# Kernel tuning notes

Hardware: AMD Instinct MI355X
Metric: run time of the kernel (lower is better)

## Reference

```python
import jax, jax.numpy as jnp
import numpy as np

NUM_HEADS = 16

def setup_inputs() -> dict:
    key = jax.random.key(0)
    ks = jax.random.split(key, 5)
    b, n, d = 2, 2048, 1024
    s = 0.02
    return {
        "x": jax.random.normal(ks[0], (b, n, d), jnp.float32),
        "wq": jax.random.normal(ks[1], (d, d), jnp.float32) * s,
        "wk": jax.random.normal(ks[2], (d, d), jnp.float32) * s,
        "wv": jax.random.normal(ks[3], (d, d), jnp.float32) * s,
        "wo": jax.random.normal(ks[4], (d, d), jnp.float32) * s,
        "bo": jnp.zeros((d,), jnp.float32),
    }

def reference(x, wq, wk, wv, wo, bo):
    b, n, c = x.shape
    h = NUM_HEADS
    hd = c // h
    scale = hd ** -0.5
    # qkv projections (qkv_bias=False); torch Linear computes x @ W.T
    def split_heads(t):
        return t.reshape(b, n, h, hd).transpose(0, 2, 1, 3)  # b h n d
    q = split_heads(x @ wq.T)
    k = split_heads(x @ wk.T)
    v = split_heads(x @ wv.T)
    dots = jnp.einsum('bhid,bhjd->bhij', q, k) * scale
    attn = jax.nn.softmax(dots, axis=-1)  # attn_drop=0 -> identity
    out = jnp.einsum('bhij,bhjd->bhid', attn, v)
    out = out.transpose(0, 2, 1, 3).reshape(b, n, c)
    out = out @ wo.T + bo  # proj_drop=0 -> identity
    return out
```

## Files before the change

kernel.cpp:

```cpp
#include <hip/hip_runtime.h>
#include <hip/hip_bf16.h>

typedef float f32x4 __attribute__((ext_vector_type(4)));
typedef short short8 __attribute__((ext_vector_type(8)));
typedef short short4v __attribute__((ext_vector_type(4)));

#define MFMA(a, b, c) __builtin_amdgcn_mfma_f32_16x16x32_bf16((a), (b), (c), 0, 0, 0)

#if __has_builtin(__builtin_amdgcn_exp2f)
#define EXP2(x) __builtin_amdgcn_exp2f(x)
#else
#define EXP2(x) exp2f(x)
#endif

#define B_  2
#define N_  2048
#define C_  1024
#define H_  16
#define HD_ 64
#define M_  (B_ * N_)

#define QSCALE 0.18033688011112042f

typedef const __attribute__((address_space(1))) void* gp_t;
typedef __attribute__((address_space(3))) void* sp_t;
#define GLL16(g, s) __builtin_amdgcn_global_load_lds((gp_t)(const void*)(g), (sp_t)(void*)(s), 16, 0, 0)

__device__ __forceinline__ short f2bf(float f) {
    union { float fv; unsigned u; } v; v.fv = f;
    unsigned r = v.u + 0x7fffu + ((v.u >> 16) & 1u);
    return (short)(r >> 16);
}
__device__ __forceinline__ unsigned pack_rne(float a, float b) {
    return (unsigned)(unsigned short)f2bf(a) | ((unsigned)(unsigned short)f2bf(b) << 16);
}

__global__ __launch_bounds__(256) void convert_kernel(
    const float* __restrict__ x,  const float* __restrict__ wq,
    const float* __restrict__ wk, const float* __restrict__ wv,
    const float* __restrict__ wo, short* __restrict__ dst)
{
    size_t e = ((size_t)blockIdx.x * 256 + threadIdx.x) * 8;
    const float* src; size_t off;
    if (e < 4194304)      { src = x;  off = e; }
    else if (e < 5242880) { src = wq; off = e - 4194304; }
    else if (e < 6291456) { src = wk; off = e - 5242880; }
    else if (e < 7340032) { src = wv; off = e - 6291456; }
    else                  { src = wo; off = e - 7340032; }
    float4 a = *(const float4*)(src + off);
    float4 b = *(const float4*)(src + off + 4);
    short8 s;
    s[0] = f2bf(a.x); s[1] = f2bf(a.y); s[2] = f2bf(a.z); s[3] = f2bf(a.w);
    s[4] = f2bf(b.x); s[5] = f2bf(b.y); s[6] = f2bf(b.z); s[7] = f2bf(b.w);
    *(short8*)(dst + e) = s;
}

__global__ __launch_bounds__(256) void qkv_gemm(
    const short* __restrict__ xb, const short* __restrict__ Wb,
    short* __restrict__ Qb, short* __restrict__ Kb, short* __restrict__ Vt)
{
    const int m0 = blockIdx.x * 128;
    const int n0 = blockIdx.y * 128;
    __shared__ short As[128 * 64];
    __shared__ short Bs[128 * 64];
    const int tid  = threadIdx.x;
    const int wave = tid >> 6, lane = tid & 63;
    const int quad = lane >> 4, l16 = lane & 15;
    const int wr = (wave >> 1) * 64, wc = (wave & 1) * 64;
    const int sw = l16 & 7;

    const int rS = tid >> 3;
    const int cS = (tid & 7) ^ (rS & 7);
    const short* A_src = xb + (size_t)(m0 + rS) * C_ + cS * 8;
    const short* B_src = Wb + (size_t)(n0 + rS) * C_ + cS * 8;

    f32x4 acc[4][4] = {};

    for (int kk = 0; kk < C_; kk += 64) {
        __syncthreads();
        #pragma unroll
        for (int it = 0; it < 4; ++it) {
            GLL16(A_src + (size_t)(it * 32) * C_ + kk, &As[it * 2048 + tid * 8]);
            GLL16(B_src + (size_t)(it * 32) * C_ + kk, &Bs[it * 2048 + tid * 8]);
        }
        __syncthreads();
        short8 af[4][2], bf[4][2];
        #pragma unroll
        for (int mi = 0; mi < 4; ++mi) {
            int row = (wr + mi * 16 + l16) * 64;
            af[mi][0] = *(const short8*)&As[row + ((quad    ) ^ sw) * 8];
            af[mi][1] = *(const short8*)&As[row + ((quad + 4) ^ sw) * 8];
        }
        #pragma unroll
        for (int ni = 0; ni < 4; ++ni) {
            int row = (wc + ni * 16 + l16) * 64;
            bf[ni][0] = *(const short8*)&Bs[row + ((quad    ) ^ sw) * 8];
            bf[ni][1] = *(const short8*)&Bs[row + ((quad + 4) ^ sw) * 8];
        }
        #pragma unroll
        for (int k2 = 0; k2 < 2; ++k2)
        #pragma unroll
        for (int mi = 0; mi < 4; ++mi)
        #pragma unroll
        for (int ni = 0; ni < 4; ++ni)
            acc[mi][ni] = MFMA(af[mi][k2], bf[ni][k2], acc[mi][ni]);
    }

    const int which = n0 >> 10;
    const int nb = n0 & 1023;
    #pragma unroll
    for (int mi = 0; mi < 4; ++mi)
    #pragma unroll
    for (int ni = 0; ni < 4; ++ni)
    #pragma unroll
    for (int r = 0; r < 4; ++r) {
        int m  = m0 + wr + mi * 16 + quad * 4 + r;
        int cc = nb + wc + ni * 16 + l16;
        float av = acc[mi][ni][r];
        if (which == 0) av *= QSCALE;
        short bv = f2bf(av);
        int bb = m >> 11, ns = m & (N_ - 1);
        int h = cc >> 6, d = cc & 63;
        size_t bh = (size_t)(bb * H_ + h);
        if (which == 0)      Qb[(bh * N_ + ns) * HD_ + d] = bv;
        else if (which == 1) Kb[(bh * N_ + ns) * HD_ + d] = bv;
        else                 Vt[(bh * HD_ + d) * N_ + ns] = bv;
    }
}

__global__ __launch_bounds__(256, 5) void attn_split(
    const short* __restrict__ Qb, const short* __restrict__ Kb,
    const short* __restrict__ Vt, float* __restrict__ Opart,
    float* __restrict__ lpart)
{
    const int bid = blockIdx.x;
    const int swz = (bid & 7) * 256 + (bid >> 3);
    const int bh = swz >> 6;
    const int i0 = ((swz >> 1) & 31) * 64;
    const int sp = swz & 1;
    __shared__ short Ks[2][64 * 64];
    __shared__ short Vs[2][64 * 64];
    const int tid  = threadIdx.x;
    const int wave = tid >> 6, lane = tid & 63;
    const int quad = lane >> 4, l16 = lane & 15;
    const int sw = l16 & 7;

    const short* Qg = Qb + ((size_t)bh * N_ + i0) * HD_;
    const short* Kg = Kb + (size_t)bh * N_ * HD_;
    const short* Vg = Vt + (size_t)bh * HD_ * N_;

    const int row0 = tid >> 3,  c0 = (tid & 7) ^ (row0 & 7);
    const int row1 = row0 + 32, c1 = (tid & 7) ^ (row1 & 7);
    const short* KgA0 = Kg + (sp * 1024 + row0) * HD_ + c0 * 8;
    const short* KgA1 = Kg + (sp * 1024 + row1) * HD_ + c1 * 8;
    const short* VgA0 = Vg + (size_t)row0 * N_ + sp * 1024 + c0 * 8;
    const short* VgA1 = Vg + (size_t)row1 * N_ + sp * 1024 + c1 * 8;

    short8 qf[2];
    {
        const short* qrow = Qg + (wave * 16 + l16) * HD_;
        qf[0] = *(const short8*)(qrow + quad * 8);
        qf[1] = *(const short8*)(qrow + quad * 8 + 32);
    }

    GLL16(KgA0, &Ks[0][tid * 8]);
    GLL16(KgA1, &Ks[0][(tid + 256) * 8]);
    GLL16(VgA0, &Vs[0][tid * 8]);
    GLL16(VgA1, &Vs[0][(tid + 256) * 8]);
    __syncthreads();

    f32x4 o[4] = {};
    float lrow = 0.f;

    for (int jt = 0; jt < 16; ++jt) {
        const int cur = jt & 1;
        if (jt + 1 < 16) {
            int j1 = (jt + 1) * 64;
            GLL16(KgA0 + (size_t)j1 * HD_, &Ks[cur ^ 1][tid * 8]);
            GLL16(KgA1 + (size_t)j1 * HD_, &Ks[cur ^ 1][(tid + 256) * 8]);
            GLL16(VgA0 + j1, &Vs[cur ^ 1][tid * 8]);
            GLL16(VgA1 + j1, &Vs[cur ^ 1][(tid + 256) * 8]);
        }
        const short* Kc = Ks[cur];
        const short* Vc = Vs[cur];

        #pragma unroll
        for (int half = 0; half < 2; ++half) {
            unsigned pq[4];
            #pragma unroll
            for (int nio = 0; nio < 2; ++nio) {
                int ni = half * 2 + nio;
                int krow = (ni * 16 + l16) * 64;
                short8 kf0 = *(const short8*)&Kc[krow + ((quad ^ sw) * 8)];
                short8 kf1 = *(const short8*)&Kc[krow + (((quad + 4) ^ sw) * 8)];
                f32x4 st = {0.f, 0.f, 0.f, 0.f};
                __builtin_amdgcn_s_setprio(1);
                st = MFMA(kf0, qf[0], st);
                st = MFMA(kf1, qf[1], st);
                __builtin_amdgcn_s_setprio(0);
                union { float f; unsigned u; } e0, e1, e2, e3;
                e0.f = EXP2(st[0]); e1.f = EXP2(st[1]);
                e2.f = EXP2(st[2]); e3.f = EXP2(st[3]);
                lrow += (e0.f + e1.f) + (e2.f + e3.f);
                pq[nio * 2]     = __builtin_amdgcn_perm(e1.u, e0.u, 0x07060302u);
                pq[nio * 2 + 1] = __builtin_amdgcn_perm(e3.u, e2.u, 0x07060302u);
            }
            #pragma unroll
            for (int di = 0; di < 4; ++di) {
                int vrow = (di * 16 + l16) * 64;
                int ch1 = (half * 4 +     (quad >> 1)) ^ sw;
                int ch2 = (half * 4 + 2 + (quad >> 1)) ^ sw;
                union { struct { short4v lo, hi; } p; short8 v; } va;
                va.p.lo = *(const short4v*)&Vc[vrow + ch1 * 8 + (quad & 1) * 4];
                va.p.hi = *(const short4v*)&Vc[vrow + ch2 * 8 + (quad & 1) * 4];
                union { unsigned u[4]; short8 v; } pb;
                pb.u[0] = pq[0]; pb.u[1] = pq[1];
                pb.u[2] = pq[2]; pb.u[3] = pq[3];
                __builtin_amdgcn_s_setprio(1);
                o[di] = MFMA(va.v, pb.v, o[di]);
                __builtin_amdgcn_s_setprio(0);
            }
        }
        __syncthreads();
    }

    {
        float l = lrow;
        l += __shfl_xor(l, 16, 64);
        l += __shfl_xor(l, 32, 64);
        int ig = i0 + wave * 16 + l16;
        float* obase = Opart + ((size_t)(sp * 32 + bh) * N_ + ig) * HD_;
        #pragma unroll
        for (int di = 0; di < 4; ++di)
            *(f32x4*)(obase + di * 16 + quad * 4) = o[di];
        if (quad == 0) lpart[sp * 65536 + bh * N_ + ig] = l;
    }
}

__global__ __launch_bounds__(256) void merge_kernel(
    const float* __restrict__ Opart, const float* __restrict__ lpart,
    short* __restrict__ Ob)
{
    int e8 = (blockIdx.x * 256 + threadIdx.x) * 8;
    int bh = e8 >> 17;
    int rem = e8 & 131071;
    int ig = rem >> 6, d = rem & 63;
    f32x4 a0 = *(const f32x4*)(Opart + e8);
    f32x4 a1 = *(const f32x4*)(Opart + e8 + 4);
    f32x4 b0 = *(const f32x4*)(Opart + 4194304 + e8);
    f32x4 b1 = *(const f32x4*)(Opart + 4194304 + e8 + 4);
    float inv = 1.f / (lpart[bh * N_ + ig] + lpart[65536 + bh * N_ + ig]);
    short8 s;
    s[0] = f2bf((a0[0] + b0[0]) * inv); s[1] = f2bf((a0[1] + b0[1]) * inv);
    s[2] = f2bf((a0[2] + b0[2]) * inv); s[3] = f2bf((a0[3] + b0[3]) * inv);
    s[4] = f2bf((a1[0] + b1[0]) * inv); s[5] = f2bf((a1[1] + b1[1]) * inv);
    s[6] = f2bf((a1[2] + b1[2]) * inv); s[7] = f2bf((a1[3] + b1[3]) * inv);
    int b = bh >> 4, h = bh & (H_ - 1);
    *(short8*)&Ob[((size_t)(b * N_ + ig)) * C_ + h * HD_ + d] = s;
}

__global__ __launch_bounds__(256) void proj_gemm(
    const short* __restrict__ Ob, const short* __restrict__ wob,
    const float* __restrict__ bo, float* __restrict__ out)
{
    const int m0 = blockIdx.x * 64;
    const int n0 = blockIdx.y * 128;
    __shared__ short As[64 * 64];
    __shared__ short Bs[128 * 64];
    const int tid  = threadIdx.x;
    const int wave = tid >> 6, lane = tid & 63;
    const int quad = lane >> 4, l16 = lane & 15;
    const int wr = (wave >> 1) * 32, wc = (wave & 1) * 64;
    const int sw = l16 & 7;

    const int rS = tid >> 3;
    const int cS = (tid & 7) ^ (rS & 7);
    const short* A_src = Ob  + (size_t)(m0 + rS) * C_ + cS * 8;
    const short* B_src = wob + (size_t)(n0 + rS) * C_ + cS * 8;

    f32x4 acc[2][4] = {};

    for (int kk = 0; kk < C_; kk += 64) {
        __syncthreads();
        GLL16(A_src + kk, &As[tid * 8]);
        GLL16(A_src + (size_t)32 * C_ + kk, &As[(tid + 256) * 8]);
        #pragma unroll
        for (int it = 0; it < 4; ++it)
            GLL16(B_src + (size_t)(it * 32) * C_ + kk, &Bs[it * 2048 + tid * 8]);
        __syncthreads();
        short8 af[2][2], bf[4][2];
        #pragma unroll
        for (int mi = 0; mi < 2; ++mi) {
            int row = (wr + mi * 16 + l16) * 64;
            af[mi][0] = *(const short8*)&As[row + ((quad    ) ^ sw) * 8];
            af[mi][1] = *(const short8*)&As[row + ((quad + 4) ^ sw) * 8];
        }
        #pragma unroll
        for (int ni = 0; ni < 4; ++ni) {
            int row = (wc + ni * 16 + l16) * 64;
            bf[ni][0] = *(const short8*)&Bs[row + ((quad    ) ^ sw) * 8];
            bf[ni][1] = *(const short8*)&Bs[row + ((quad + 4) ^ sw) * 8];
        }
        #pragma unroll
        for (int k2 = 0; k2 < 2; ++k2)
        #pragma unroll
        for (int mi = 0; mi < 2; ++mi)
        #pragma unroll
        for (int ni = 0; ni < 4; ++ni)
            acc[mi][ni] = MFMA(af[mi][k2], bf[ni][k2], acc[mi][ni]);
    }

    #pragma unroll
    for (int mi = 0; mi < 2; ++mi)
    #pragma unroll
    for (int ni = 0; ni < 4; ++ni)
    #pragma unroll
    for (int r = 0; r < 4; ++r) {
        int m = m0 + wr + mi * 16 + quad * 4 + r;
        int c = n0 + wc + ni * 16 + l16;
        out[(size_t)m * C_ + c] = acc[mi][ni][r] + bo[c];
    }
}

extern "C" void kernel_launch(void* const* d_in, const int* in_sizes, int n_in,
                              void* d_out, int out_size, void* d_ws, size_t ws_size,
                              hipStream_t stream) {
    const float* x  = (const float*)d_in[0];
    const float* wq = (const float*)d_in[1];
    const float* wk = (const float*)d_in[2];
    const float* wv = (const float*)d_in[3];
    const float* wo = (const float*)d_in[4];
    const float* bo = (const float*)d_in[5];
    float* out = (float*)d_out;

    short* xb  = (short*)d_ws;
    short* Wb  = xb  + 4194304;
    short* wob = Wb  + 3145728;
    short* Qb  = wob + 1048576;
    short* Kb  = Qb  + 4194304;
    short* Vt  = Kb  + 4194304;
    short* Obuf= Vt  + 4194304;
    float* Opart = (float*)(Obuf + 4194304);
    float* lpart = Opart + 2 * 4194304;

    dim3 blk(256);
    convert_kernel<<<4096, blk, 0, stream>>>(x, wq, wk, wv, wo, xb);
    qkv_gemm<<<dim3(M_ / 128, 3072 / 128), blk, 0, stream>>>(xb, Wb, Qb, Kb, Vt);
    attn_split<<<2048, blk, 0, stream>>>(Qb, Kb, Vt, Opart, lpart);
    merge_kernel<<<2048, blk, 0, stream>>>(Opart, lpart, Obuf);
    proj_gemm<<<dim3(M_ / 64, C_ / 128), blk, 0, stream>>>(Obuf, wob, bo, out);
}
```

Baseline: 197.0 us.

## Process two 16-row query subtiles per wave to reuse K/V fragments

Each wave in the split attention kernel now handles 32 query rows (two 16-row subtiles) instead of 16, so each block covers 128 query rows and the grid shrinks from 2048 to 1024 blocks. K and V fragments read from shared memory are reused across both subtiles. This halves the global-to-LDS traffic for K/V per query row and the number of LDS fragment reads per MFMA. In exchange it raises register pressure (occupancy hint lowered from 5 to 4) and leaves fewer blocks to fill the GPU.

```diff
diff --git a/kernel.cpp b/kernel.cpp
--- a/kernel.cpp
+++ b/kernel.cpp
@@ -128,15 +128,15 @@
     }
 }
 
-__global__ __launch_bounds__(256, 5) void attn_split(
+__global__ __launch_bounds__(256, 4) void attn_split(
     const short* __restrict__ Qb, const short* __restrict__ Kb,
     const short* __restrict__ Vt, float* __restrict__ Opart,
     float* __restrict__ lpart)
 {
     const int bid = blockIdx.x;
-    const int swz = (bid & 7) * 256 + (bid >> 3);
-    const int bh = swz >> 6;
-    const int i0 = ((swz >> 1) & 31) * 64;
+    const int swz = (bid & 7) * 128 + (bid >> 3);
+    const int bh = swz >> 5;
+    const int i0 = ((swz >> 1) & 15) * 128;
     const int sp = swz & 1;
     __shared__ short Ks[2][64 * 64];
     __shared__ short Vs[2][64 * 64];
@@ -156,11 +156,12 @@
     const short* VgA0 = Vg + (size_t)row0 * N_ + sp * 1024 + c0 * 8;
     const short* VgA1 = Vg + (size_t)row1 * N_ + sp * 1024 + c1 * 8;
 
-    short8 qf[2];
-    {
-        const short* qrow = Qg + (wave * 16 + l16) * HD_;
-        qf[0] = *(const short8*)(qrow + quad * 8);
-        qf[1] = *(const short8*)(qrow + quad * 8 + 32);
+    short8 qf[2][2];
+    #pragma unroll
+    for (int s = 0; s < 2; ++s) {
+        const short* qrow = Qg + (wave * 32 + s * 16 + l16) * HD_;
+        qf[s][0] = *(const short8*)(qrow + quad * 8);
+        qf[s][1] = *(const short8*)(qrow + quad * 8 + 32);
     }
 
     GLL16(KgA0, &Ks[0][tid * 8]);
@@ -169,8 +170,8 @@
     GLL16(VgA1, &Vs[0][(tid + 256) * 8]);
     __syncthreads();
 
-    f32x4 o[4] = {};
-    float lrow = 0.f;
+    f32x4 o[2][4] = {};
+    float lrow[2] = {0.f, 0.f};
 
     for (int jt = 0; jt < 16; ++jt) {
         const int cur = jt & 1;
@@ -186,24 +187,27 @@
 
         #pragma unroll
         for (int half = 0; half < 2; ++half) {
-            unsigned pq[4];
+            unsigned pq[2][4];
             #pragma unroll
             for (int nio = 0; nio < 2; ++nio) {
                 int ni = half * 2 + nio;
                 int krow = (ni * 16 + l16) * 64;
                 short8 kf0 = *(const short8*)&Kc[krow + ((quad ^ sw) * 8)];
                 short8 kf1 = *(const short8*)&Kc[krow + (((quad + 4) ^ sw) * 8)];
-                f32x4 st = {0.f, 0.f, 0.f, 0.f};
-                __builtin_amdgcn_s_setprio(1);
-                st = MFMA(kf0, qf[0], st);
-                st = MFMA(kf1, qf[1], st);
-                __builtin_amdgcn_s_setprio(0);
-                union { float f; unsigned u; } e0, e1, e2, e3;
-                e0.f = EXP2(st[0]); e1.f = EXP2(st[1]);
-                e2.f = EXP2(st[2]); e3.f = EXP2(st[3]);
-                lrow += (e0.f + e1.f) + (e2.f + e3.f);
-                pq[nio * 2]     = __builtin_amdgcn_perm(e1.u, e0.u, 0x07060302u);
-                pq[nio * 2 + 1] = __builtin_amdgcn_perm(e3.u, e2.u, 0x07060302u);
+                #pragma unroll
+                for (int s = 0; s < 2; ++s) {
+                    f32x4 st = {0.f, 0.f, 0.f, 0.f};
+                    __builtin_amdgcn_s_setprio(1);
+                    st = MFMA(kf0, qf[s][0], st);
+                    st = MFMA(kf1, qf[s][1], st);
+                    __builtin_amdgcn_s_setprio(0);
+                    union { float f; unsigned u; } e0, e1, e2, e3;
+                    e0.f = EXP2(st[0]); e1.f = EXP2(st[1]);
+                    e2.f = EXP2(st[2]); e3.f = EXP2(st[3]);
+                    lrow[s] += (e0.f + e1.f) + (e2.f + e3.f);
+                    pq[s][nio * 2]     = __builtin_amdgcn_perm(e1.u, e0.u, 0x07060302u);
+                    pq[s][nio * 2 + 1] = __builtin_amdgcn_perm(e3.u, e2.u, 0x07060302u);
+                }
             }
             #pragma unroll
             for (int di = 0; di < 4; ++di) {
@@ -213,26 +217,30 @@
                 union { struct { short4v lo, hi; } p; short8 v; } va;
                 va.p.lo = *(const short4v*)&Vc[vrow + ch1 * 8 + (quad & 1) * 4];
                 va.p.hi = *(const short4v*)&Vc[vrow + ch2 * 8 + (quad & 1) * 4];
-                union { unsigned u[4]; short8 v; } pb;
-                pb.u[0] = pq[0]; pb.u[1] = pq[1];
-                pb.u[2] = pq[2]; pb.u[3] = pq[3];
                 __builtin_amdgcn_s_setprio(1);
-                o[di] = MFMA(va.v, pb.v, o[di]);
+                #pragma unroll
+                for (int s = 0; s < 2; ++s) {
+                    union { unsigned u[4]; short8 v; } pb;
+                    pb.u[0] = pq[s][0]; pb.u[1] = pq[s][1];
+                    pb.u[2] = pq[s][2]; pb.u[3] = pq[s][3];
+                    o[s][di] = MFMA(va.v, pb.v, o[s][di]);
+                }
                 __builtin_amdgcn_s_setprio(0);
             }
         }
         __syncthreads();
     }
 
-    {
-        float l = lrow;
+    #pragma unroll
+    for (int s = 0; s < 2; ++s) {
+        float l = lrow[s];
         l += __shfl_xor(l, 16, 64);
         l += __shfl_xor(l, 32, 64);
-        int ig = i0 + wave * 16 + l16;
+        int ig = i0 + wave * 32 + s * 16 + l16;
         float* obase = Opart + ((size_t)(sp * 32 + bh) * N_ + ig) * HD_;
         #pragma unroll
         for (int di = 0; di < 4; ++di)
-            *(f32x4*)(obase + di * 16 + quad * 4) = o[di];
+            *(f32x4*)(obase + di * 16 + quad * 4) = o[s][di];
         if (quad == 0) lpart[sp * 65536 + bh * N_ + ig] = l;
     }
 }
@@ -346,7 +354,7 @@
     dim3 blk(256);
     convert_kernel<<<4096, blk, 0, stream>>>(x, wq, wk, wv, wo, xb);
     qkv_gemm<<<dim3(M_ / 128, 3072 / 128), blk, 0, stream>>>(xb, Wb, Qb, Kb, Vt);
-    attn_split<<<2048, blk, 0, stream>>>(Qb, Kb, Vt, Opart, lpart);
+    attn_split<<<1024, blk, 0, stream>>>(Qb, Kb, Vt, Opart, lpart);
     merge_kernel<<<2048, blk, 0, stream>>>(Opart, lpart, Obuf);
     proj_gemm<<<dim3(M_ / 64, C_ / 128), blk, 0, stream>>>(Obuf, wob, bo, out);
 }
```

After: 190.7 us. -3.2%, faster.
